# Kernel optimization log

Hardware: AMD Instinct MI355X
Metric: run time of the kernel (lower is better)

Reference implementation:

```python
import jax, jax.numpy as jnp
import numpy as np

B, S, D, H, HD, F = 2, 2048, 2048, 16, 128, 8192
EPS = 1e-5
THETA = 10000.0
NEG = -1e30


def _rmsnorm(x, w):
    v = jnp.mean(jnp.square(x.astype(jnp.float32)), axis=-1, keepdims=True)
    return (x.astype(jnp.float32) * jax.lax.rsqrt(v + EPS)).astype(x.dtype) * w


def _rope(x):
    # x: [B, S, H, HD]; llama-style rotate-half rotary embedding
    inv_freq = 1.0 / (THETA ** (jnp.arange(0, HD, 2, dtype=jnp.float32) / HD))
    ang = jnp.arange(S, dtype=jnp.float32)[:, None] * inv_freq[None, :]  # [S, HD//2]
    cos = jnp.concatenate([jnp.cos(ang), jnp.cos(ang)], axis=-1)[None, :, None, :]
    sin = jnp.concatenate([jnp.sin(ang), jnp.sin(ang)], axis=-1)[None, :, None, :]
    x1, x2 = jnp.split(x, 2, axis=-1)
    return x * cos + jnp.concatenate([-x2, x1], axis=-1) * sin


def _mlp(x, wg, wu, wd):
    # SiLU-gated HiggsAudioMLP: down(silu(gate(x)) * up(x))
    return (jax.nn.silu(x @ wg) * (x @ wu)) @ wd


def setup_inputs() -> dict:
    key = jax.random.key(0)
    ks = jax.random.split(key, 12)
    std = 0.02
    p = lambda k, shape: jax.random.normal(k, shape, dtype=jnp.float32) * std
    return {
        "hidden_states": jax.random.normal(ks[0], (B, S, D), dtype=jnp.float32),
        "audio_out_mask": jax.random.randint(ks[1], (B, S), 0, 2).astype(bool),
        "wq": p(ks[2], (D, H * HD)),
        "wk": p(ks[3], (D, H * HD)),
        "wv": p(ks[4], (D, H * HD)),
        "wo": p(ks[5], (H * HD, D)),
        "input_ln_w": jnp.ones((D,), jnp.float32),
        "post_ln_w": jnp.ones((D,), jnp.float32),
        "audio_post_ln_w": jnp.ones((D,), jnp.float32),
        "w_gate_t": p(ks[6], (D, F)),
        "w_up_t": p(ks[7], (D, F)),
        "w_down_t": p(ks[8], (F, D)),
        "w_gate_a": p(ks[9], (D, F)),
        "w_up_a": p(ks[10], (D, F)),
        "w_down_a": p(ks[11], (F, D)),
    }


def reference(hidden_states, audio_out_mask, wq, wk, wv, wo, input_ln_w, post_ln_w,
              audio_post_ln_w, w_gate_t, w_up_t, w_down_t, w_gate_a, w_up_a, w_down_a):
    # ---- self-attention block ----
    residual = hidden_states
    h = _rmsnorm(hidden_states, input_ln_w)
    q = _rope((h @ wq).reshape(B, S, H, HD))
    k = _rope((h @ wk).reshape(B, S, H, HD))
    v = (h @ wv).reshape(B, S, H, HD)
    scores = jnp.einsum("bqhd,bkhd->bhqk", q, k) / float(np.sqrt(HD))
    causal = jnp.tril(jnp.ones((S, S), bool))
    scores = jnp.where(causal[None, None], scores, NEG)
    attn = jax.nn.softmax(scores, axis=-1)
    ctx = jnp.einsum("bhqk,bkhd->bqhd", attn, v).reshape(B, S, H * HD)
    hidden_states = residual + ctx @ wo
    # ---- dual FFN, per-token routed by audio_out_mask ----
    residual = hidden_states
    text_out = _mlp(_rmsnorm(hidden_states, post_ln_w), w_gate_t, w_up_t, w_down_t)
    audio_out = _mlp(_rmsnorm(hidden_states, audio_post_ln_w), w_gate_a, w_up_a, w_down_a)
    return residual + jnp.where(audio_out_mask[..., None], audio_out, text_out)
```

## Files before the change

### kernel.cpp

```cpp
#include <hip/hip_runtime.h>


#define BB 2
#define SS 2048
#define DD 2048
#define HH 16
#define HDD 128
#define FF 8192
#define TT (BB*SS)
#define RPAD 4608

typedef unsigned short ushort_t;
typedef __bf16 bf16x8 __attribute__((ext_vector_type(8)));
typedef float f32x4 __attribute__((ext_vector_type(4)));

#define DEV static __device__ __forceinline__

DEV float bf2f(ushort_t u) { __bf16 b; __builtin_memcpy(&b, &u, 2); return (float)b; }
DEV ushort_t f2bf(float f) { __bf16 b = (__bf16)f; ushort_t u; __builtin_memcpy(&u, &b, 2); return u; }

DEV void gl_lds16(const ushort_t* g, ushort_t* l) {
    __builtin_amdgcn_global_load_lds((const __attribute__((address_space(1))) void*)g,
                                     (__attribute__((address_space(3))) void*)l, 16, 0, 0);
}

#define BARRIER() do { asm volatile("" ::: "memory"); __builtin_amdgcn_s_barrier(); asm volatile("" ::: "memory"); } while (0)
#define LGKM0()   asm volatile("s_waitcnt lgkmcnt(0)" ::: "memory")

struct ConvSeg { const float* in; ushort_t* out; int K, N, cumEnd; };
struct ConvArgs { ConvSeg s[10]; };

__global__ __launch_bounds__(256) void prep_all(ConvArgs a, int convEnd,
                                                float2* __restrict__ cstab,
                                                const float* __restrict__ hs,
                                                const float* __restrict__ iln,
                                                ushort_t* __restrict__ h_bf,
                                                const unsigned char* __restrict__ raw,
                                                int* __restrict__ perm,
                                                int* __restrict__ header) {
    __shared__ float t[32][33];
    const int bid = blockIdx.x;
    const int tid = threadIdx.x;
    if (bid < convEnd) {
        int i = 0;
        while (bid >= a.s[i].cumEnd) ++i;
        const int base = (i == 0) ? 0 : a.s[i - 1].cumEnd;
        const int local = bid - base;
        const float* __restrict__ in = a.s[i].in;
        ushort_t* __restrict__ out = a.s[i].out;
        const int K = a.s[i].K, N = a.s[i].N;
        const int ntile = N >> 5;
        const int n0 = (local % ntile) * 32, k0 = (local / ntile) * 32;
        const int tx = tid & 31, ty = tid >> 5;
#pragma unroll
        for (int j = 0; j < 4; ++j)
            t[ty + 8 * j][tx] = in[(size_t)(k0 + ty + 8 * j) * N + n0 + tx];
        __syncthreads();
#pragma unroll
        for (int j = 0; j < 4; ++j)
            out[(size_t)(n0 + ty + 8 * j) * K + k0 + tx] = f2bf(t[tx][ty + 8 * j]);
    } else if (bid < convEnd + 512) {
        const int idx = (bid - convEnd) * 256 + tid;
        const int s = idx >> 6, i = idx & 63;
        const float inv = powf(10000.0f, -(float)i * (1.0f / 64.0f));
        const float ang = (float)s * inv;
        cstab[idx] = make_float2(cosf(ang), sinf(ang));
    } else if (bid < convEnd + 512 + TT) {
        const int row = bid - convEnd - 512;
        const float4* xr = (const float4*)(hs + (size_t)row * DD);
        float4 v0 = xr[tid * 2], v1 = xr[tid * 2 + 1];
        float ss = v0.x * v0.x + v0.y * v0.y + v0.z * v0.z + v0.w * v0.w
                 + v1.x * v1.x + v1.y * v1.y + v1.z * v1.z + v1.w * v1.w;
#pragma unroll
        for (int d = 1; d < 64; d <<= 1) ss += __shfl_xor(ss, d);
        float* red = &t[0][0];
        if ((tid & 63) == 0) red[tid >> 6] = ss;
        __syncthreads();
        const float tot = red[0] + red[1] + red[2] + red[3];
        const float sc = rsqrtf(tot * (1.0f / DD) + 1e-5f);
        const float4* wr = (const float4*)iln;
        float4 w0 = wr[tid * 2], w1 = wr[tid * 2 + 1];
        ushort_t* o = h_bf + (size_t)row * DD + tid * 8;
        o[0] = f2bf(v0.x * sc * w0.x); o[1] = f2bf(v0.y * sc * w0.y);
        o[2] = f2bf(v0.z * sc * w0.z); o[3] = f2bf(v0.w * sc * w0.w);
        o[4] = f2bf(v1.x * sc * w1.x); o[5] = f2bf(v1.y * sc * w1.y);
        o[6] = f2bf(v1.z * sc * w1.z); o[7] = f2bf(v1.w * sc * w1.w);
    } else {
        int* ip = (int*)&t[0][0];
        int* ct = ip;
        int* ca = ip + 256;
        int* st = ip + 512;
        int* sa = ip + 768;
        int* misc = ip + 1024;
        if (tid == 0) misc[0] = 0;
        __syncthreads();
        int any = 0;
        for (int i = tid; i < TT; i += 256)
            if ((i & 3) != 0 && raw[i] != 0) any = 1;
        if (any) atomicOr(&misc[0], 1);
        __syncthreads();
        const int is_byte = misc[0];
        auto mget = [&](int r) -> int {
            return is_byte ? (raw[r] != 0) : (((const int*)raw)[r] != 0);
        };
        int c0 = 0, c1 = 0;
#pragma unroll
        for (int i = 0; i < 16; ++i) {
            if (mget(tid * 16 + i)) c1++; else c0++;
        }
        ct[tid] = c0; ca[tid] = c1;
        __syncthreads();
        if (tid == 0) {
            int at = 0, aa = 0;
            for (int i = 0; i < 256; ++i) {
                st[i] = at; at += ct[i];
                sa[i] = aa; aa += ca[i];
            }
            misc[1] = at; misc[2] = aa;
        }
        __syncthreads();
        const int Nt = misc[1], Na = misc[2];
        const int A0 = (Nt + 255) & ~255;
        const int live = A0 + ((Na + 255) & ~255);
        int pt = st[tid], pa = A0 + sa[tid];
#pragma unroll
        for (int i = 0; i < 16; ++i) {
            const int r = tid * 16 + i;
            if (mget(r)) perm[pa++] = r; else perm[pt++] = r;
        }
        for (int i = Nt + tid; i < A0; i += 256) perm[i] = -1;
        for (int i = A0 + Na + tid; i < RPAD; i += 256) perm[i] = -1;
        if (tid == 0) { header[0] = Nt; header[1] = A0; header[2] = Na; header[3] = live; }
    }
}

__global__ __launch_bounds__(256) void rmsnorm_gather(const float* __restrict__ x,
                                                      const float* __restrict__ wt_text,
                                                      const float* __restrict__ wt_audio,
                                                      const int* __restrict__ perm,
                                                      const int* __restrict__ header,
                                                      ushort_t* __restrict__ out) {
    const int i = blockIdx.x, tid = threadIdx.x;
    const int p = perm[i];
    ushort_t* o = out + (size_t)i * DD + tid * 8;
    if (p < 0) {
#pragma unroll
        for (int j = 0; j < 8; ++j) o[j] = 0;
        return;
    }
    const float* wt = (i < header[1]) ? wt_text : wt_audio;
    const float4* xr = (const float4*)(x + (size_t)p * DD);
    float4 v0 = xr[tid * 2], v1 = xr[tid * 2 + 1];
    float ss = v0.x * v0.x + v0.y * v0.y + v0.z * v0.z + v0.w * v0.w
             + v1.x * v1.x + v1.y * v1.y + v1.z * v1.z + v1.w * v1.w;
#pragma unroll
    for (int d = 1; d < 64; d <<= 1) ss += __shfl_xor(ss, d);
    __shared__ float red[4];
    if ((tid & 63) == 0) red[tid >> 6] = ss;
    __syncthreads();
    const float tot = red[0] + red[1] + red[2] + red[3];
    const float sc = rsqrtf(tot * (1.0f / DD) + 1e-5f);
    const float4* wr = (const float4*)wt;
    float4 w0 = wr[tid * 2], w1 = wr[tid * 2 + 1];
    o[0] = f2bf(v0.x * sc * w0.x); o[1] = f2bf(v0.y * sc * w0.y);
    o[2] = f2bf(v0.z * sc * w0.z); o[3] = f2bf(v0.w * sc * w0.w);
    o[4] = f2bf(v1.x * sc * w1.x); o[5] = f2bf(v1.y * sc * w1.y);
    o[6] = f2bf(v1.z * sc * w1.z); o[7] = f2bf(v1.w * sc * w1.w);
}

template <int EPI>
__global__ __launch_bounds__(512, 2) void gemm_nt8(
    const ushort_t* __restrict__ A, const ushort_t* __restrict__ W,
    int K, ushort_t* __restrict__ o0, ushort_t* __restrict__ o1,
    ushort_t* __restrict__ o2, float* __restrict__ Cf,
    const float* __restrict__ resid, const float2* __restrict__ cstab) {
    const int nwg = gridDim.x * gridDim.y;
    int bid = blockIdx.y * gridDim.x + blockIdx.x;
    bid = (bid & 7) * (nwg >> 3) + (bid >> 3);
    const int bxx = bid % gridDim.x;
    const int byy = bid / gridDim.x;
    const int m0 = byy * 256;
    int kind = 0, n0;
    const ushort_t* B;
    if (EPI == 0) {
        kind = bxx >> 4;
        n0 = (bxx & 15) * 128;
        B = W + (size_t)kind * DD * DD + (size_t)n0 * K;
    } else {
        n0 = bxx * 128;
        B = W + (size_t)n0 * K;
    }
    __shared__ ushort_t smem[49152];
    const int tid = threadIdx.x;
    const int w = tid >> 6, lane = tid & 63;
    const int wm = w >> 2, wn = w & 3;
    const int f16 = lane & 15, g4 = lane >> 4;
    const int rl = tid >> 3;
    const int cc8 = (((tid & 7) ^ ((tid >> 3) & 7)) * 8);
    const ushort_t* gA = A + (size_t)m0 * K;

    auto stageAq = [&](int buf, int k0, int q) {
        gl_lds16(gA + (size_t)(q * 64 + rl) * K + k0 + cc8,
                 &smem[buf * 24576 + q * 4096 + w * 512]);
    };
    auto stageB2 = [&](int buf, int k0) {
#pragma unroll
        for (int j = 0; j < 2; ++j)
            gl_lds16(B + (size_t)(j * 64 + rl) * K + k0 + cc8,
                     &smem[buf * 24576 + 16384 + j * 4096 + w * 512]);
    };

    const int aBase = (wm * 128 + f16) * 64;
    const int bBase = (wn * 32 + f16) * 64;
    int cswz[2];
    cswz[0] = ((g4 ^ (f16 & 7)) * 8);
    cswz[1] = (((4 + g4) ^ (f16 & 7)) * 8);

    f32x4 acc[8][2] = {};
    bf16x8 af[4][2], bfr[2][2];

    stageAq(0, 0, 0); stageAq(0, 0, 1); stageAq(0, 0, 2); stageAq(0, 0, 3);
    stageB2(0, 0);
    stageAq(1, 64, 0); stageAq(1, 64, 2); stageB2(1, 64);
    asm volatile("s_waitcnt vmcnt(4)" ::: "memory");
    BARRIER();

    const int nt = K / 64;
    for (int t = 0; t < nt; ++t) {
        const int cur = t & 1;
        const int ab = cur * 24576, bb = cur * 24576 + 16384;
#pragma unroll
        for (int m = 0; m < 4; ++m)
#pragma unroll
            for (int ks = 0; ks < 2; ++ks)
                af[m][ks] = *(const bf16x8*)&smem[ab + aBase + m * 1024 + cswz[ks]];
#pragma unroll
        for (int np = 0; np < 2; ++np)
#pragma unroll
            for (int ks = 0; ks < 2; ++ks)
                bfr[np][ks] = *(const bf16x8*)&smem[bb + bBase + np * 1024 + cswz[ks]];
        if (t + 1 < nt) {
            stageAq(1 - cur, (t + 1) * 64, 1);
            stageAq(1 - cur, (t + 1) * 64, 3);
        }
        BARRIER();
        LGKM0();
        __builtin_amdgcn_s_setprio(1);
#pragma unroll
        for (int m = 0; m < 4; ++m)
#pragma unroll
            for (int np = 0; np < 2; ++np)
#pragma unroll
                for (int ks = 0; ks < 2; ++ks)
                    acc[m][np] = __builtin_amdgcn_mfma_f32_16x16x32_bf16(af[m][ks], bfr[np][ks], acc[m][np], 0, 0, 0);
        __builtin_amdgcn_s_setprio(0);
        BARRIER();
#pragma unroll
        for (int m = 0; m < 4; ++m)
#pragma unroll
            for (int ks = 0; ks < 2; ++ks)
                af[m][ks] = *(const bf16x8*)&smem[ab + aBase + (4 + m) * 1024 + cswz[ks]];
        if (t + 2 < nt) {
            stageAq(cur, (t + 2) * 64, 0);
            stageAq(cur, (t + 2) * 64, 2);
            stageB2(cur, (t + 2) * 64);
        }
        BARRIER();
        LGKM0();
        __builtin_amdgcn_s_setprio(1);
#pragma unroll
        for (int m = 0; m < 4; ++m)
#pragma unroll
            for (int np = 0; np < 2; ++np)
#pragma unroll
                for (int ks = 0; ks < 2; ++ks)
                    acc[4 + m][np] = __builtin_amdgcn_mfma_f32_16x16x32_bf16(af[m][ks], bfr[np][ks], acc[4 + m][np], 0, 0, 0);
        __builtin_amdgcn_s_setprio(0);
        if (t + 2 < nt) { asm volatile("s_waitcnt vmcnt(4)" ::: "memory"); }
        else            { asm volatile("s_waitcnt vmcnt(0)" ::: "memory"); }
        BARRIER();
    }

    if (EPI == 0 && kind <= 1) {
        ushort_t* outp = (kind == 0) ? o0 : o1;
        __syncthreads();
#pragma unroll
        for (int m = 0; m < 8; ++m)
#pragma unroll
            for (int np = 0; np < 2; ++np)
#pragma unroll
                for (int j = 0; j < 4; ++j)
                    smem[(wm * 128 + m * 16 + g4 * 4 + j) * 128 + wn * 32 + np * 16 + f16]
                        = f2bf(acc[m][np][j]);
        __syncthreads();
#pragma unroll
        for (int m = 0; m < 8; ++m)
#pragma unroll
            for (int j = 0; j < 4; ++j) {
                const int rloc = wm * 128 + m * 16 + g4 * 4 + j;
                const int r = m0 + rloc;
                const int s = r & (SS - 1);
#pragma unroll
                for (int np = 0; np < 2; ++np) {
                    const int d = wn * 32 + np * 16 + f16;
                    const float2 cs = cstab[s * 64 + (d & 63)];
                    const float v = acc[m][np][j];
                    const float p = bf2f(smem[rloc * 128 + (d ^ 64)]);
                    const float out = (d < 64) ? (v * cs.x - p * cs.y)
                                               : (v * cs.x + p * cs.y);
                    outp[(size_t)r * DD + n0 + d] = f2bf(out);
                }
            }
    } else {
#pragma unroll
        for (int m = 0; m < 8; ++m)
#pragma unroll
            for (int np = 0; np < 2; ++np)
#pragma unroll
                for (int j = 0; j < 4; ++j) {
                    const int r = m0 + wm * 128 + m * 16 + g4 * 4 + j;
                    const int c = n0 + wn * 32 + np * 16 + f16;
                    const float v = acc[m][np][j];
                    if (EPI == 0) {
                        const int b = r >> 11, s = r & (SS - 1), h = c >> 7, d = c & 127;
                        o2[(((size_t)(b * HH + h) * HDD + d) << 11) + s] = f2bf(v);
                    } else {
                        const size_t idx = (size_t)r * DD + c;
                        Cf[idx] = resid[idx] + v;
                    }
                }
    }
}

__global__ __launch_bounds__(256, 2) void gemm_down_c(
    const ushort_t* __restrict__ A, const ushort_t* __restrict__ Bt_text,
    const ushort_t* __restrict__ Bt_audio, float* __restrict__ C,
    const int* __restrict__ perm, const int* __restrict__ header) {
    const int nwg = gridDim.x * gridDim.y;
    int bid = blockIdx.y * gridDim.x + blockIdx.x;
    bid = (bid & 7) * (nwg >> 3) + (bid >> 3);
    const int m0 = (bid / gridDim.x) * 128;
    if (m0 >= header[3]) return;
    const ushort_t* Bt = (m0 >= header[1]) ? Bt_audio : Bt_text;
    __shared__ ushort_t As[128 * 32];
    __shared__ ushort_t Bs[128 * 32];
    const int tid = threadIdx.x;
    const int w = tid >> 6, lane = tid & 63;
    const int n0 = (bid % gridDim.x) * 128;
    const int wr = w >> 1, wc = w & 1;
    f32x4 acc[4][4] = {};
    const ushort_t* gA = A + (size_t)m0 * FF;
    const ushort_t* gB = Bt + (size_t)n0 * FF;
    const int c0 = tid, c1 = 256 + tid;
    const int r0 = c0 >> 2, o0 = (c0 & 3) * 8;
    const int r1 = c1 >> 2, o1 = (c1 & 3) * 8;
    ushort_t* lA0 = &As[(w * 64) * 8];
    ushort_t* lA1 = &As[(256 + w * 64) * 8];
    ushort_t* lB0 = &Bs[(w * 64) * 8];
    ushort_t* lB1 = &Bs[(256 + w * 64) * 8];
    for (int k0 = 0; k0 < FF; k0 += 32) {
        __syncthreads();
        gl_lds16(gA + (size_t)r0 * FF + k0 + o0, lA0);
        gl_lds16(gA + (size_t)r1 * FF + k0 + o1, lA1);
        gl_lds16(gB + (size_t)r0 * FF + k0 + o0, lB0);
        gl_lds16(gB + (size_t)r1 * FF + k0 + o1, lB1);
        asm volatile("s_waitcnt vmcnt(0)" ::: "memory");
        __syncthreads();
        const int ko = (lane >> 4) * 8;
        const int ra = wr * 64 + (lane & 15);
        const int rb = wc * 64 + (lane & 15);
        bf16x8 af[4], bfv[4];
#pragma unroll
        for (int mi = 0; mi < 4; ++mi) af[mi] = *(const bf16x8*)&As[(ra + mi * 16) * 32 + ko];
#pragma unroll
        for (int ni = 0; ni < 4; ++ni) bfv[ni] = *(const bf16x8*)&Bs[(rb + ni * 16) * 32 + ko];
#pragma unroll
        for (int mi = 0; mi < 4; ++mi)
#pragma unroll
            for (int ni = 0; ni < 4; ++ni)
                acc[mi][ni] = __builtin_amdgcn_mfma_f32_16x16x32_bf16(af[mi], bfv[ni], acc[mi][ni], 0, 0, 0);
    }
    const int cl = lane & 15, r4 = (lane >> 4) * 4;
#pragma unroll
    for (int mi = 0; mi < 4; ++mi)
#pragma unroll
        for (int ni = 0; ni < 4; ++ni)
#pragma unroll
            for (int j = 0; j < 4; ++j) {
                const int r = m0 + wr * 64 + mi * 16 + r4 + j;
                const int p = perm[r];
                if (p >= 0) {
                    const int c = n0 + wc * 64 + ni * 16 + cl;
                    float* q = C + (size_t)p * DD + c;
                    *q = *q + acc[mi][ni][j];
                }
            }
}

__global__ __launch_bounds__(512, 2) void gemm_gu8(
    const ushort_t* __restrict__ A,
    const ushort_t* __restrict__ Bg_t, const ushort_t* __restrict__ Bu_t,
    const ushort_t* __restrict__ Bg_a, const ushort_t* __restrict__ Bu_a,
    ushort_t* __restrict__ act, const int* __restrict__ header) {
    const int nwg = gridDim.x * gridDim.y;
    int bid = blockIdx.y * gridDim.x + blockIdx.x;
    bid = (bid & 7) * (nwg >> 3) + (bid >> 3);
    const int bx = bid % 64;
    const int by = bid / 64;
    const int m0 = by * 256;
    if (m0 >= header[3]) return;
    const bool audio = (m0 >= header[1]);
    const ushort_t* Bg = audio ? Bg_a : Bg_t;
    const ushort_t* Bu = audio ? Bu_a : Bu_t;
    const int n0g = bx * 128;

    __shared__ ushort_t smem[65536];
    const int tid = threadIdx.x;
    const int w = tid >> 6, lane = tid & 63;
    const int wm = w >> 2, wn = w & 3;
    const int f16 = lane & 15, g4 = lane >> 4;

    const int rl = tid >> 3;
    const int cc8 = (((tid & 7) ^ ((tid >> 3) & 7)) * 8);
    const int wchunk = w * 64;

    const ushort_t* gA = A + (size_t)m0 * DD;

    auto stageA_h = [&](int buf, int k0, int h) {
#pragma unroll
        for (int j = 0; j < 2; ++j) {
            const int r = h * 128 + j * 64 + rl;
            gl_lds16(gA + (size_t)r * DD + k0 + cc8,
                     &smem[buf * 32768 + h * 8192 + (j * 512 + wchunk) * 8]);
        }
    };
    auto stageB_h = [&](int buf, int k0, int h) {
#pragma unroll
        for (int j = 0; j < 2; ++j) {
            const int br = h * 128 + j * 64 + rl;
            const int ty = (br >> 4) & 1;
            const int grow = ((br >> 5) << 4) + (br & 15);
            const ushort_t* src = (ty ? Bu : Bg) + (size_t)(n0g + grow) * DD + k0 + cc8;
            gl_lds16(src, &smem[buf * 32768 + 16384 + h * 8192 + (j * 512 + wchunk) * 8]);
        }
    };

    const int aBase = (wm * 128 + f16) * 64;
    const int bBase = (wn * 64 + f16) * 64;
    int cswz[2];
    cswz[0] = ((g4 ^ (f16 & 7)) * 8);
    cswz[1] = (((4 + g4) ^ (f16 & 7)) * 8);

    f32x4 acc[8][4] = {};
    bf16x8 af[4][2], b0[2][2], b1[2][2];

    stageA_h(0, 0, 0); stageA_h(0, 0, 1);
    stageB_h(0, 0, 0); stageB_h(0, 0, 1);
    stageA_h(1, 64, 0); stageB_h(1, 64, 0);
    asm volatile("s_waitcnt vmcnt(4)" ::: "memory");
    BARRIER();

    const int nt = DD / 64;
    for (int t = 0; t < nt; ++t) {
        const int buf = t & 1, obuf = buf ^ 1;
        const int ab = buf * 32768, bb = buf * 32768 + 16384;
        const int k1 = (t + 1) * 64, k2 = (t + 2) * 64;
        const bool pf1 = (t + 1) < nt, pf2 = (t + 2) < nt;
#pragma unroll
        for (int m = 0; m < 4; ++m)
#pragma unroll
            for (int ks = 0; ks < 2; ++ks)
                af[m][ks] = *(const bf16x8*)&smem[ab + aBase + m * 1024 + cswz[ks]];
#pragma unroll
        for (int n = 0; n < 2; ++n)
#pragma unroll
            for (int ks = 0; ks < 2; ++ks)
                b0[n][ks] = *(const bf16x8*)&smem[bb + bBase + n * 1024 + cswz[ks]];
        if (pf1) stageA_h(obuf, k1, 1);
        BARRIER();
        LGKM0();
        __builtin_amdgcn_s_setprio(1);
#pragma unroll
        for (int m = 0; m < 4; ++m)
#pragma unroll
            for (int n = 0; n < 2; ++n)
#pragma unroll
                for (int ks = 0; ks < 2; ++ks)
                    acc[m][n] = __builtin_amdgcn_mfma_f32_16x16x32_bf16(af[m][ks], b0[n][ks], acc[m][n], 0, 0, 0);
        __builtin_amdgcn_s_setprio(0);
        BARRIER();
#pragma unroll
        for (int n = 0; n < 2; ++n)
#pragma unroll
            for (int ks = 0; ks < 2; ++ks)
                b1[n][ks] = *(const bf16x8*)&smem[bb + bBase + (2 + n) * 1024 + cswz[ks]];
        if (pf1) stageB_h(obuf, k1, 1);
        BARRIER();
        LGKM0();
        __builtin_amdgcn_s_setprio(1);
#pragma unroll
        for (int m = 0; m < 4; ++m)
#pragma unroll
            for (int n = 0; n < 2; ++n)
#pragma unroll
                for (int ks = 0; ks < 2; ++ks)
                    acc[m][2 + n] = __builtin_amdgcn_mfma_f32_16x16x32_bf16(af[m][ks], b1[n][ks], acc[m][2 + n], 0, 0, 0);
        __builtin_amdgcn_s_setprio(0);
        BARRIER();
#pragma unroll
        for (int m = 0; m < 4; ++m)
#pragma unroll
            for (int ks = 0; ks < 2; ++ks)
                af[m][ks] = *(const bf16x8*)&smem[ab + aBase + (4 + m) * 1024 + cswz[ks]];
        if (pf2) stageB_h(buf, k2, 0);
        BARRIER();
        LGKM0();
        __builtin_amdgcn_s_setprio(1);
#pragma unroll
        for (int m = 0; m < 4; ++m)
#pragma unroll
            for (int n = 0; n < 2; ++n)
#pragma unroll
                for (int ks = 0; ks < 2; ++ks)
                    acc[4 + m][n] = __builtin_amdgcn_mfma_f32_16x16x32_bf16(af[m][ks], b0[n][ks], acc[4 + m][n], 0, 0, 0);
        __builtin_amdgcn_s_setprio(0);
        BARRIER();
        if (pf2) stageA_h(buf, k2, 0);
        BARRIER();
        __builtin_amdgcn_s_setprio(1);
#pragma unroll
        for (int m = 0; m < 4; ++m)
#pragma unroll
            for (int n = 0; n < 2; ++n)
#pragma unroll
                for (int ks = 0; ks < 2; ++ks)
                    acc[4 + m][2 + n] = __builtin_amdgcn_mfma_f32_16x16x32_bf16(af[m][ks], b1[n][ks], acc[4 + m][2 + n], 0, 0, 0);
        __builtin_amdgcn_s_setprio(0);
        if (pf2)      { asm volatile("s_waitcnt vmcnt(4)" ::: "memory"); }
        else if (pf1) { asm volatile("s_waitcnt vmcnt(0)" ::: "memory"); }
        BARRIER();
    }

    const int r4 = g4 * 4;
#pragma unroll
    for (int m = 0; m < 8; ++m)
#pragma unroll
        for (int np = 0; np < 2; ++np) {
            const int f = n0g + (wn * 2 + np) * 16 + f16;
#pragma unroll
            for (int j = 0; j < 4; ++j) {
                const int r = m0 + wm * 128 + m * 16 + r4 + j;
                const float g = acc[m][np * 2][j], u = acc[m][np * 2 + 1][j];
                act[(size_t)r * FF + f] = f2bf(g / (1.0f + __expf(-g)) * u);
            }
        }
}

__global__ __launch_bounds__(512, 4) void attn_k(
    const ushort_t* __restrict__ qb, const ushort_t* __restrict__ kb,
    const ushort_t* __restrict__ vt, ushort_t* __restrict__ ctx) {
    __shared__ ushort_t Ks[2][64 * 128];
    __shared__ ushort_t Vs[128 * 64];
    __shared__ ushort_t Pw[8][16 * 64];
    const int tid = threadIdx.x, w = tid >> 6, lane = tid & 63;
    const int qt = gridDim.x - 1 - blockIdx.x;
    const int bh = blockIdx.y, b = bh >> 4, h = bh & 15;
    const int q0 = qt * 128 + w * 16;
    const int f16 = lane & 15, g4 = lane >> 4;
    bf16x8 aq[4];
    {
        const ushort_t* qr = qb + ((size_t)(b * SS + q0 + f16)) * DD + h * HDD + g4 * 8;
#pragma unroll
        for (int ko = 0; ko < 4; ++ko) aq[ko] = *(const bf16x8*)(qr + ko * 32);
    }
    auto stageK = [&](int bufi, int kt) {
        const int sk0 = kt * 64;
#pragma unroll
        for (int i = 0; i < 2; ++i) {
            const int c = i * 512 + tid;
            const int csrc = ((c & 15) ^ ((c >> 4) & 7)) * 8;
            gl_lds16(kb + ((size_t)(b * SS + sk0 + (c >> 4))) * DD + h * HDD + csrc,
                     &Ks[bufi][(i * 512 + w * 64) * 8]);
        }
    };
    auto stageV = [&](int kt) {
        const int sk0 = kt * 64;
#pragma unroll
        for (int i = 0; i < 2; ++i) {
            const int c = i * 512 + tid;
            const int csrc = ((c & 7) ^ ((c >> 3) & 7)) * 8;
            gl_lds16(vt + ((size_t)((b * HH + h) * HDD + (c >> 3))) * SS + sk0 + csrc,
                     &Vs[(i * 512 + w * 64) * 8]);
        }
    };
    f32x4 o[8] = {};
    float mrow[4] = {-3e38f, -3e38f, -3e38f, -3e38f};
    float lrow[4] = {};
    const int nkv = 2 * qt + 2;
    stageK(0, 0); stageV(0);
    asm volatile("s_waitcnt vmcnt(0)" ::: "memory");
    BARRIER();
    for (int kt = 0; kt < nkv; ++kt) {
        const int cur = kt & 1;
        const bool pf = (kt + 1 < nkv);
        if (pf) stageK(cur ^ 1, kt + 1);
        f32x4 s[4] = {};
        __builtin_amdgcn_s_setprio(1);
#pragma unroll
        for (int ko = 0; ko < 4; ++ko)
#pragma unroll
            for (int ni = 0; ni < 4; ++ni) {
                bf16x8 bk = *(const bf16x8*)&Ks[cur][(ni * 16 + f16) * 128 + (((ko * 4 + g4) ^ (f16 & 7)) * 8)];
                s[ni] = __builtin_amdgcn_mfma_f32_16x16x32_bf16(aq[ko], bk, s[ni], 0, 0, 0);
            }
        __builtin_amdgcn_s_setprio(0);
        const float scale = 0.08838834764831843f;
#pragma unroll
        for (int ni = 0; ni < 4; ++ni)
#pragma unroll
            for (int j = 0; j < 4; ++j) {
                float v = s[ni][j] * scale;
                const int kg = kt * 64 + ni * 16 + f16;
                const int qg = q0 + g4 * 4 + j;
                if (kg > qg) v = -1e30f;
                s[ni][j] = v;
            }
#pragma unroll
        for (int j = 0; j < 4; ++j) {
            float tm = fmaxf(fmaxf(s[0][j], s[1][j]), fmaxf(s[2][j], s[3][j]));
#pragma unroll
            for (int dd = 1; dd < 16; dd <<= 1) tm = fmaxf(tm, __shfl_xor(tm, dd));
            if (!__all(tm <= mrow[j] + 8.0f)) {
                const float mn = fmaxf(mrow[j], tm);
                const float corr = __expf(mrow[j] - mn);
                lrow[j] *= corr;
#pragma unroll
                for (int di = 0; di < 8; ++di) o[di][j] *= corr;
                mrow[j] = mn;
            }
            float sum = 0.f;
#pragma unroll
            for (int ni = 0; ni < 4; ++ni) {
                const float p = __expf(s[ni][j] - mrow[j]);
                s[ni][j] = p;
                sum += p;
            }
#pragma unroll
            for (int dd = 1; dd < 16; dd <<= 1) sum += __shfl_xor(sum, dd);
            lrow[j] += sum;
        }
#pragma unroll
        for (int ni = 0; ni < 4; ++ni)
#pragma unroll
            for (int j = 0; j < 4; ++j) {
                const int prow = g4 * 4 + j;
                const int pcb = ni * 2 + (f16 >> 3);
                Pw[w][prow * 64 + ((pcb ^ (prow & 7)) * 8) + (f16 & 7)] = f2bf(s[ni][j]);
            }
        if (pf) { asm volatile("s_waitcnt vmcnt(2)" ::: "memory"); }
        else    { asm volatile("s_waitcnt vmcnt(0)" ::: "memory"); }
        BARRIER();
        __builtin_amdgcn_s_setprio(1);
#pragma unroll
        for (int ks = 0; ks < 2; ++ks) {
            bf16x8 pa = *(const bf16x8*)&Pw[w][f16 * 64 + (((ks * 4 + g4) ^ (f16 & 7)) * 8)];
#pragma unroll
            for (int di = 0; di < 8; ++di) {
                bf16x8 bv = *(const bf16x8*)&Vs[(di * 16 + f16) * 64 + (((ks * 4 + g4) ^ (f16 & 7)) * 8)];
                o[di] = __builtin_amdgcn_mfma_f32_16x16x32_bf16(pa, bv, o[di], 0, 0, 0);
            }
        }
        __builtin_amdgcn_s_setprio(0);
        BARRIER();
        if (pf) {
            stageV(kt + 1);
            asm volatile("s_waitcnt vmcnt(2)" ::: "memory");
        }
        BARRIER();
    }
    float inv[4];
#pragma unroll
    for (int j = 0; j < 4; ++j) inv[j] = 1.0f / lrow[j];
#pragma unroll
    for (int di = 0; di < 8; ++di)
#pragma unroll
        for (int j = 0; j < 4; ++j) {
            const int r = q0 + g4 * 4 + j;
            ctx[((size_t)(b * SS + r)) * DD + h * HDD + di * 16 + f16] = f2bf(o[di][j] * inv[j]);
        }
}

extern "C" void kernel_launch(void* const* d_in, const int* in_sizes, int n_in,
                              void* d_out, int out_size, void* d_ws, size_t ws_size,
                              hipStream_t stream) {
    (void)in_sizes; (void)n_in; (void)out_size; (void)ws_size;
    const float* hs  = (const float*)d_in[0];
    const unsigned char* mask_raw = (const unsigned char*)d_in[1];
    const float* wq  = (const float*)d_in[2];
    const float* wk  = (const float*)d_in[3];
    const float* wv  = (const float*)d_in[4];
    const float* wo  = (const float*)d_in[5];
    const float* iln = (const float*)d_in[6];
    const float* pln = (const float*)d_in[7];
    const float* aln = (const float*)d_in[8];
    const float* wgt = (const float*)d_in[9];
    const float* wut = (const float*)d_in[10];
    const float* wdt = (const float*)d_in[11];
    const float* wga = (const float*)d_in[12];
    const float* wua = (const float*)d_in[13];
    const float* wda = (const float*)d_in[14];

    const size_t SZ_W1 = (size_t)DD * DD * 2;
    const size_t SZ_W2 = (size_t)DD * FF * 2;
    const size_t SZ_A  = (size_t)TT * DD * 2;

    char* ws = (char*)d_ws;
    size_t off = 0;
    auto take = [&](size_t n) { char* p = ws + off; off += n; return p; };
    ushort_t* wq_t  = (ushort_t*)take(SZ_W1);
    ushort_t* wk_t  = (ushort_t*)take(SZ_W1);
    ushort_t* wv_t  = (ushort_t*)take(SZ_W1);
    ushort_t* wo_t  = (ushort_t*)take(SZ_W1);
    ushort_t* wg_tb = (ushort_t*)take(SZ_W2);
    ushort_t* wu_tb = (ushort_t*)take(SZ_W2);
    ushort_t* wd_tb = (ushort_t*)take(SZ_W2);
    ushort_t* wg_ab = (ushort_t*)take(SZ_W2);
    ushort_t* wu_ab = (ushort_t*)take(SZ_W2);
    ushort_t* wd_ab = (ushort_t*)take(SZ_W2);
    char* actreg = take(6 * SZ_A);
    float2* cstab = (float2*)take((size_t)SS * 64 * 8);
    int* perm   = (int*)take(RPAD * 4);
    int* header = (int*)take(64);

    ushort_t* h_bf = (ushort_t*)(actreg);
    ushort_t* qb   = (ushort_t*)(actreg + 1 * SZ_A);
    ushort_t* kb   = (ushort_t*)(actreg + 2 * SZ_A);
    ushort_t* vt   = (ushort_t*)(actreg + 3 * SZ_A);
    ushort_t* ctx  = (ushort_t*)(actreg + 4 * SZ_A);
    ushort_t* hn_c  = (ushort_t*)(actreg);
    ushort_t* act_c = (ushort_t*)(actreg + (size_t)RPAD * DD * 2);

    const dim3 blk(256);

    ConvArgs ca;
    int cum = 0;
    auto seg = [&](int i, const float* in, ushort_t* out, int K, int N) {
        cum += (N / 32) * (K / 32);
        ca.s[i] = ConvSeg{in, out, K, N, cum};
    };
    seg(0, wq, wq_t, DD, DD);
    seg(1, wk, wk_t, DD, DD);
    seg(2, wv, wv_t, DD, DD);
    seg(3, wo, wo_t, DD, DD);
    seg(4, wgt, wg_tb, DD, FF);
    seg(5, wut, wu_tb, DD, FF);
    seg(6, wdt, wd_tb, FF, DD);
    seg(7, wga, wg_ab, DD, FF);
    seg(8, wua, wu_ab, DD, FF);
    seg(9, wda, wd_ab, FF, DD);
    prep_all<<<cum + 512 + TT + 1, blk, 0, stream>>>(ca, cum, cstab, hs, iln, h_bf,
                                                     mask_raw, perm, header);

    gemm_nt8<0><<<dim3(48, TT / 256), dim3(512), 0, stream>>>(
        h_bf, wq_t, DD, qb, kb, vt, nullptr, nullptr, cstab);
    attn_k<<<dim3(SS / 128, BB * HH), dim3(512), 0, stream>>>(qb, kb, vt, ctx);
    gemm_nt8<1><<<dim3(DD / 128, TT / 256), dim3(512), 0, stream>>>(
        ctx, wo_t, DD, nullptr, nullptr, nullptr, (float*)d_out, hs, nullptr);

    rmsnorm_gather<<<RPAD, blk, 0, stream>>>((const float*)d_out, pln, aln, perm, header, hn_c);
    gemm_gu8<<<dim3(FF / 128, RPAD / 256), dim3(512), 0, stream>>>(hn_c, wg_tb, wu_tb, wg_ab, wu_ab, act_c, header);
    gemm_down_c<<<dim3(DD / 128, RPAD / 128), blk, 0, stream>>>(act_c, wd_tb, wd_ab, (float*)d_out, perm, header);
}
```

Measured before the change: 979.5 us.

## Restructure gate/up GEMM into four-quadrant ping-pong with per-phase prefetch

Replaces the gate/up MLP GEMM main loop's three-stage staggered prefetch schedule with a four-phase loop. In each phase a wave computes one quadrant of its tile (a half of M by a half of N) and issues one quarter of the next k-tile's loads into the other buffer. The wave-to-tile mapping moves from a 2x4 grid of 128x64 tiles to interleaved quadrants, and the epilogue is rewritten to match. The aim is a simpler, more even overlap of global-to-LDS loads with MFMA work. The cost is an extra vmcnt wait and two barriers every phase, plus reloading A fragments for each quadrant, which adds LDS reads.

Measured after the change: 1.007 ms. 1.03x slower.

```diff
diff --git a/kernel.cpp b/kernel.cpp
--- a/kernel.cpp
+++ b/kernel.cpp
@@ -417,7 +417,7 @@
     __shared__ ushort_t smem[65536];
     const int tid = threadIdx.x;
     const int w = tid >> 6, lane = tid & 63;
-    const int wm = w >> 2, wn = w & 3;
+    const int wm2 = w >> 2, wn4 = w & 3;
     const int f16 = lane & 15, g4 = lane >> 4;
 
     const int rl = tid >> 3;
@@ -445,115 +445,80 @@
         }
     };
 
-    const int aBase = (wm * 128 + f16) * 64;
-    const int bBase = (wn * 64 + f16) * 64;
     int cswz[2];
     cswz[0] = ((g4 ^ (f16 & 7)) * 8);
     cswz[1] = (((4 + g4) ^ (f16 & 7)) * 8);
 
-    f32x4 acc[8][4] = {};
-    bf16x8 af[4][2], b0[2][2], b1[2][2];
-
-    stageA_h(0, 0, 0); stageA_h(0, 0, 1);
-    stageB_h(0, 0, 0); stageB_h(0, 0, 1);
-    stageA_h(1, 64, 0); stageB_h(1, 64, 0);
-    asm volatile("s_waitcnt vmcnt(4)" ::: "memory");
+    f32x4 acc[4][4][2] = {};
+    bf16x8 af[4][2], bfv[2][2];
+
+    stageA_h(0, 0, 0); stageB_h(0, 0, 0);
+    asm volatile("s_waitcnt vmcnt(0)" ::: "memory");
+    stageB_h(0, 0, 1); stageA_h(0, 0, 1);
     BARRIER();
 
     const int nt = DD / 64;
     for (int t = 0; t < nt; ++t) {
         const int buf = t & 1, obuf = buf ^ 1;
         const int ab = buf * 32768, bb = buf * 32768 + 16384;
-        const int k1 = (t + 1) * 64, k2 = (t + 2) * 64;
-        const bool pf1 = (t + 1) < nt, pf2 = (t + 2) < nt;
+        const int k1 = (t + 1) * 64;
+        const bool pf = (t + 1) < nt;
+#pragma unroll
+        for (int p = 0; p < 4; ++p) {
+            const int mh = (p >= 2) ? 1 : 0;
+            const int nh = (p == 1 || p == 2) ? 1 : 0;
+            const int aB = ab + (mh * 128 + wm2 * 64 + f16) * 64;
+            const int bB = bb + (nh * 128 + wn4 * 32 + f16) * 64;
+#pragma unroll
+            for (int m = 0; m < 4; ++m)
+#pragma unroll
+                for (int ks = 0; ks < 2; ++ks)
+                    af[m][ks] = *(const bf16x8*)&smem[aB + m * 1024 + cswz[ks]];
+#pragma unroll
+            for (int n = 0; n < 2; ++n)
+#pragma unroll
+                for (int ks = 0; ks < 2; ++ks)
+                    bfv[n][ks] = *(const bf16x8*)&smem[bB + n * 1024 + cswz[ks]];
+            if (pf) {
+                if (p == 0)      stageA_h(obuf, k1, 0);
+                else if (p == 1) stageB_h(obuf, k1, 0);
+                else if (p == 2) stageB_h(obuf, k1, 1);
+                else             stageA_h(obuf, k1, 1);
+                asm volatile("s_waitcnt vmcnt(4)" ::: "memory");
+            } else {
+                asm volatile("s_waitcnt vmcnt(0)" ::: "memory");
+            }
+            BARRIER();
+            LGKM0();
+            __builtin_amdgcn_s_setprio(1);
+#pragma unroll
+            for (int m = 0; m < 4; ++m)
+#pragma unroll
+                for (int n = 0; n < 2; ++n)
+#pragma unroll
+                    for (int ks = 0; ks < 2; ++ks)
+                        acc[p][m][n] = __builtin_amdgcn_mfma_f32_16x16x32_bf16(
+                            af[m][ks], bfv[n][ks], acc[p][m][n], 0, 0, 0);
+            __builtin_amdgcn_s_setprio(0);
+            BARRIER();
+        }
+    }
+
+#pragma unroll
+    for (int p = 0; p < 4; ++p) {
+        const int mh = (p >= 2) ? 1 : 0;
+        const int nh = (p == 1 || p == 2) ? 1 : 0;
+        const int brg = nh * 128 + wn4 * 32 + f16;
+        const int f = n0g + ((brg >> 5) << 4) + (brg & 15);
 #pragma unroll
         for (int m = 0; m < 4; ++m)
 #pragma unroll
-            for (int ks = 0; ks < 2; ++ks)
-                af[m][ks] = *(const bf16x8*)&smem[ab + aBase + m * 1024 + cswz[ks]];
-#pragma unroll
-        for (int n = 0; n < 2; ++n)
-#pragma unroll
-            for (int ks = 0; ks < 2; ++ks)
-                b0[n][ks] = *(const bf16x8*)&smem[bb + bBase + n * 1024 + cswz[ks]];
-        if (pf1) stageA_h(obuf, k1, 1);
-        BARRIER();
-        LGKM0();
-        __builtin_amdgcn_s_setprio(1);
-#pragma unroll
-        for (int m = 0; m < 4; ++m)
-#pragma unroll
-            for (int n = 0; n < 2; ++n)
-#pragma unroll
-                for (int ks = 0; ks < 2; ++ks)
-                    acc[m][n] = __builtin_amdgcn_mfma_f32_16x16x32_bf16(af[m][ks], b0[n][ks], acc[m][n], 0, 0, 0);
-        __builtin_amdgcn_s_setprio(0);
-        BARRIER();
-#pragma unroll
-        for (int n = 0; n < 2; ++n)
-#pragma unroll
-            for (int ks = 0; ks < 2; ++ks)
-                b1[n][ks] = *(const bf16x8*)&smem[bb + bBase + (2 + n) * 1024 + cswz[ks]];
-        if (pf1) stageB_h(obuf, k1, 1);
-        BARRIER();
-        LGKM0();
-        __builtin_amdgcn_s_setprio(1);
-#pragma unroll
-        for (int m = 0; m < 4; ++m)
-#pragma unroll
-            for (int n = 0; n < 2; ++n)
-#pragma unroll
-                for (int ks = 0; ks < 2; ++ks)
-                    acc[m][2 + n] = __builtin_amdgcn_mfma_f32_16x16x32_bf16(af[m][ks], b1[n][ks], acc[m][2 + n], 0, 0, 0);
-        __builtin_amdgcn_s_setprio(0);
-        BARRIER();
-#pragma unroll
-        for (int m = 0; m < 4; ++m)
-#pragma unroll
-            for (int ks = 0; ks < 2; ++ks)
-                af[m][ks] = *(const bf16x8*)&smem[ab + aBase + (4 + m) * 1024 + cswz[ks]];
-        if (pf2) stageB_h(buf, k2, 0);
-        BARRIER();
-        LGKM0();
-        __builtin_amdgcn_s_setprio(1);
-#pragma unroll
-        for (int m = 0; m < 4; ++m)
-#pragma unroll
-            for (int n = 0; n < 2; ++n)
-#pragma unroll
-                for (int ks = 0; ks < 2; ++ks)
-                    acc[4 + m][n] = __builtin_amdgcn_mfma_f32_16x16x32_bf16(af[m][ks], b0[n][ks], acc[4 + m][n], 0, 0, 0);
-        __builtin_amdgcn_s_setprio(0);
-        BARRIER();
-        if (pf2) stageA_h(buf, k2, 0);
-        BARRIER();
-        __builtin_amdgcn_s_setprio(1);
-#pragma unroll
-        for (int m = 0; m < 4; ++m)
-#pragma unroll
-            for (int n = 0; n < 2; ++n)
-#pragma unroll
-                for (int ks = 0; ks < 2; ++ks)
-                    acc[4 + m][2 + n] = __builtin_amdgcn_mfma_f32_16x16x32_bf16(af[m][ks], b1[n][ks], acc[4 + m][2 + n], 0, 0, 0);
-        __builtin_amdgcn_s_setprio(0);
-        if (pf2)      { asm volatile("s_waitcnt vmcnt(4)" ::: "memory"); }
-        else if (pf1) { asm volatile("s_waitcnt vmcnt(0)" ::: "memory"); }
-        BARRIER();
-    }
-
-    const int r4 = g4 * 4;
-#pragma unroll
-    for (int m = 0; m < 8; ++m)
-#pragma unroll
-        for (int np = 0; np < 2; ++np) {
-            const int f = n0g + (wn * 2 + np) * 16 + f16;
-#pragma unroll
             for (int j = 0; j < 4; ++j) {
-                const int r = m0 + wm * 128 + m * 16 + r4 + j;
-                const float g = acc[m][np * 2][j], u = acc[m][np * 2 + 1][j];
+                const int r = m0 + mh * 128 + wm2 * 64 + m * 16 + g4 * 4 + j;
+                const float g = acc[p][m][0][j], u = acc[p][m][1][j];
                 act[(size_t)r * FF + f] = f2bf(g / (1.0f + __expf(-g)) * u);
             }
-        }
+    }
 }
 
 __global__ __launch_bounds__(512, 4) void attn_k(
```
